# Kernel tuning notes

Hardware: AMD Instinct MI355X
Metric: run time of the kernel (lower is better)

## Reference

```python
import jax, jax.numpy as jnp
from jax import lax
import numpy as np

T, B, D, H = 512, 256, 128, 256
SHIFT = 0.0


def setup_inputs() -> dict:
    key = jax.random.key(0)
    ks = jax.random.split(key, 11)
    s_in = 1.0 / np.sqrt(D + H)
    s_cl = 1.0 / np.sqrt(H)
    return {
        "inputs": jax.random.normal(ks[0], (T, B, D), dtype=jnp.float32),
        "Wf": jax.random.normal(ks[1], (H, D + H), dtype=jnp.float32) * s_in,
        "bf": jax.random.normal(ks[2], (H,), dtype=jnp.float32) * s_in,
        "Wi": jax.random.normal(ks[3], (H, D + H), dtype=jnp.float32) * s_in,
        "bi": jax.random.normal(ks[4], (H,), dtype=jnp.float32) * s_in,
        "Wg": jax.random.normal(ks[5], (H, D + H), dtype=jnp.float32) * s_in,
        "bg": jax.random.normal(ks[6], (H,), dtype=jnp.float32) * s_in,
        "Wo": jax.random.normal(ks[7], (H, D + H), dtype=jnp.float32) * s_in,
        "bo": jax.random.normal(ks[8], (H,), dtype=jnp.float32) * s_in,
        "Wc": jax.random.normal(ks[9], (1, H), dtype=jnp.float32) * s_cl,
        "bc": jax.random.normal(ks[10], (1,), dtype=jnp.float32) * s_cl,
    }


def reference(inputs, Wf, bf, Wi, bi, Wg, bg, Wo, bo, Wc, bc):
    # Fuse the four gate linears into one GEMM per step: [4H, D+H]
    W = jnp.concatenate([Wf, Wi, Wg, Wo], axis=0)
    b = jnp.concatenate([bf, bi, bg, bo], axis=0)
    h = W.shape[0] // 4
    batch = inputs.shape[1]

    def step(carry, x):
        hx, cx = carry
        combined = jnp.concatenate([x, hx], axis=1)      # [B, D+H]
        z = combined @ W.T + b                            # [B, 4H]
        f = jax.nn.sigmoid(z[:, 0 * h:1 * h])
        i = jax.nn.sigmoid(z[:, 1 * h:2 * h])
        g = jnp.tanh(z[:, 2 * h:3 * h])
        o = jax.nn.sigmoid(z[:, 3 * h:4 * h])
        cx = f * cx + i * g
        hx = o * jnp.tanh(cx)
        return (hx, cx), hx

    h0 = jnp.zeros((batch, h), dtype=inputs.dtype)
    c0 = jnp.zeros((batch, h), dtype=inputs.dtype)
    (hx, cx), hs = lax.scan(step, (h0, c0), inputs)       # hs: [T, B, H]

    logits = hs @ Wc.T + bc                               # [T, B, 1]
    probs = jax.nn.sigmoid(logits + SHIFT)
    return (jnp.concatenate([probs, 1.0 - probs], axis=-1), hx, cx)
```

## Files before the change

### kernel.cpp

```cpp
#include <hip/hip_runtime.h>
#include <hip/hip_bf16.h>


#define T_STEPS 512
#define BATCH   256
#define DIN     128
#define HID     256
#define KDIM    384
#define LDK     520
#define GRIDN   256
#define NPOLL   96

typedef __attribute__((ext_vector_type(8))) short short8;
typedef __attribute__((ext_vector_type(4))) short short4v;
typedef __attribute__((ext_vector_type(4))) float f32x4;

__device__ __forceinline__ unsigned short f2bf(float f) {
    unsigned u = __float_as_uint(f);
    unsigned r = (u + 0x7FFFu + ((u >> 16) & 1u)) >> 16;
    return (unsigned short)r;
}
__device__ __forceinline__ float bf2f(unsigned short s) {
    return __uint_as_float(((unsigned)s) << 16);
}
__device__ __forceinline__ float sigmoid_f(float x) {
    return 1.f / (1.f + __expf(-x));
}
__device__ __forceinline__ float tanh_f(float x) {
    float e = __expf(2.f * x);
    return 1.f - 2.f / (e + 1.f);
}
__device__ __forceinline__ void poll_load_sc0(const unsigned int* p, uint4& a,
                                              uint4& b, uint4& c, uint4& d) {
    asm volatile(
        "global_load_dwordx4 %0, %4, off sc0\n\t"
        "global_load_dwordx4 %1, %4, off offset:16 sc0\n\t"
        "global_load_dwordx4 %2, %4, off offset:32 sc0\n\t"
        "global_load_dwordx4 %3, %4, off offset:48 sc0\n\t"
        "s_waitcnt vmcnt(0)"
        : "=&v"(a), "=&v"(b), "=&v"(c), "=&v"(d) : "v"(p) : "memory");
}
__device__ __forceinline__ void poll_load_sc1(const unsigned int* p, uint4& a,
                                              uint4& b, uint4& c, uint4& d) {
    asm volatile(
        "global_load_dwordx4 %0, %4, off sc1\n\t"
        "global_load_dwordx4 %1, %4, off offset:16 sc1\n\t"
        "global_load_dwordx4 %2, %4, off offset:32 sc1\n\t"
        "global_load_dwordx4 %3, %4, off offset:48 sc1\n\t"
        "s_waitcnt vmcnt(0)"
        : "=&v"(a), "=&v"(b), "=&v"(c), "=&v"(d) : "v"(p) : "memory");
}
__device__ __forceinline__ void store_sc0_u32(unsigned int* p, unsigned int v) {
    asm volatile("global_store_dword %0, %1, off sc0" :: "v"(p), "v"(v) : "memory");
}
__device__ __forceinline__ void store_sc1_u32(unsigned int* p, unsigned int v) {
    asm volatile("global_store_dword %0, %1, off sc1" :: "v"(p), "v"(v) : "memory");
}
__device__ __forceinline__ unsigned pack2bf(unsigned lo, unsigned hi) {
    return (hi & 0xFFFF0000u) | (lo >> 16);
}
__device__ __forceinline__ bool tags_ok(const uint4& a, const uint4& b,
                                        const uint4& c, const uint4& d,
                                        unsigned tag) {
    return ((a.x ^ tag) & 0xFFFFu) == 0 && ((a.y ^ tag) & 0xFFFFu) == 0 &&
           ((a.z ^ tag) & 0xFFFFu) == 0 && ((a.w ^ tag) & 0xFFFFu) == 0 &&
           ((b.x ^ tag) & 0xFFFFu) == 0 && ((b.y ^ tag) & 0xFFFFu) == 0 &&
           ((b.z ^ tag) & 0xFFFFu) == 0 && ((b.w ^ tag) & 0xFFFFu) == 0 &&
           ((c.x ^ tag) & 0xFFFFu) == 0 && ((c.y ^ tag) & 0xFFFFu) == 0 &&
           ((c.z ^ tag) & 0xFFFFu) == 0 && ((c.w ^ tag) & 0xFFFFu) == 0 &&
           ((d.x ^ tag) & 0xFFFFu) == 0 && ((d.y ^ tag) & 0xFFFFu) == 0 &&
           ((d.z ^ tag) & 0xFFFFu) == 0 && ((d.w ^ tag) & 0xFFFFu) == 0;
}

__global__ __launch_bounds__(256) void pack_w(
    const float* __restrict__ Wf, const float* __restrict__ Wi,
    const float* __restrict__ Wg, const float* __restrict__ Wo,
    unsigned short* __restrict__ Wp) {
    int idx = blockIdx.x * 256 + threadIdx.x;
    int n = idx / KDIM;
    int k = idx - n * KDIM;
    int g = n >> 8, j = n & 255;
    const float* s = (g == 0) ? Wf : (g == 1) ? Wi : (g == 2) ? Wg : Wo;
    Wp[idx] = f2bf(s[j * KDIM + k]);
}

__global__ __launch_bounds__(256) void pack_b(
    const float* __restrict__ bf, const float* __restrict__ bi,
    const float* __restrict__ bg, const float* __restrict__ bo,
    float* __restrict__ bp) {
    int n = blockIdx.x * 256 + threadIdx.x;
    int g = n >> 8, j = n & 255;
    const float* s = (g == 0) ? bf : (g == 1) ? bi : (g == 2) ? bg : bo;
    bp[n] = s[j];
}

__global__ __launch_bounds__(256) void init_k(unsigned int* __restrict__ hxp) {
    int tid = blockIdx.x * 256 + threadIdx.x;
    hxp[tid] = 0u;
    hxp[65536 + tid] = 0u;
    hxp[131072 + tid] = 0u;
    hxp[196608 + tid] = 0u;
}

__global__ __launch_bounds__(256, 1) void lstm_persist(
    const float* __restrict__ X,
    const unsigned short* __restrict__ W,
    const float* __restrict__ bias,
    unsigned int* __restrict__ hxp,
    unsigned short* __restrict__ hist,
    float* __restrict__ out) {
    __shared__ __align__(16) unsigned short comb_s[16 * LDK];
    __shared__ __align__(16) float z_s[4 * 272];
    __shared__ __align__(16) char pad_s[46080];
    __shared__ int fastok_s;

    const int tid = threadIdx.x;
    const int bg = blockIdx.x & 15, jg = blockIdx.x >> 4;
    const int b0 = bg * 16, j0 = jg * 16;
    const int wave = tid >> 6, lane = tid & 63;
    const int l16 = lane & 15, quad = lane >> 4;
    const int bi = tid >> 4, jj = tid & 15;
    const int b = b0 + bi, j = j0 + jj;

    const unsigned short* wrow =
        W + (size_t)(wave * 256 + j0 + l16) * KDIM + quad * 8;
    short8 wb[12];
#pragma unroll
    for (int kt = 0; kt < 12; ++kt) wb[kt] = *(const short8*)(wrow + kt * 32);

    const float bs0 = bias[0 * HID + j];
    const float bs1 = bias[1 * HID + j];
    const float bs2 = bias[2 * HID + j];
    const float bs3 = bias[3 * HID + j];
    if (tid == 0) {
        fastok_s = 1;
        ((volatile char*)pad_s)[0] = 0;
    }

    float c_reg = 0.f;
    float h_final = 0.f;

    const unsigned short* arow = &comb_s[l16 * LDK + quad * 8];
    const int hrow = tid >> 4, hc = tid & 15;
    const int xr0 = tid >> 5, xc4 = tid & 31, xr1 = (tid + 256) >> 5;

    {
        const float* x0b = X + b0 * DIN;
        float4 t0 = *(const float4*)(x0b + xr0 * DIN + xc4 * 4);
        float4 t1 = *(const float4*)(x0b + xr1 * DIN + xc4 * 4);
        short4v r;
        r.x = (short)f2bf(t0.x); r.y = (short)f2bf(t0.y);
        r.z = (short)f2bf(t0.z); r.w = (short)f2bf(t0.w);
        *(short4v*)(&comb_s[xr0 * LDK + xc4 * 4]) = r;
        r.x = (short)f2bf(t1.x); r.y = (short)f2bf(t1.y);
        r.z = (short)f2bf(t1.z); r.w = (short)f2bf(t1.w);
        *(short4v*)(&comb_s[xr1 * LDK + xc4 * 4]) = r;
    }
    float4 xv0 = *(const float4*)(X + (size_t)BATCH * DIN + b0 * DIN + xr0 * DIN + xc4 * 4);
    float4 xv1 = *(const float4*)(X + (size_t)BATCH * DIN + b0 * DIN + xr1 * DIN + xc4 * 4);
    __syncthreads();

    f32x4 acc_x0 = {0.f, 0.f, 0.f, 0.f}, acc_x1 = {0.f, 0.f, 0.f, 0.f};
#pragma unroll
    for (int kp = 0; kp < 2; ++kp) {
        short8 a0 = *(const short8*)(arow + (2 * kp) * 32);
        short8 a1 = *(const short8*)(arow + (2 * kp + 1) * 32);
        acc_x0 = __builtin_amdgcn_mfma_f32_16x16x32_bf16(a0, wb[2 * kp], acc_x0, 0, 0, 0);
        acc_x1 = __builtin_amdgcn_mfma_f32_16x16x32_bf16(a1, wb[2 * kp + 1], acc_x1, 0, 0, 0);
    }

    for (int k = 0; k < T_STEPS; ++k) {
        const unsigned tag = (unsigned)k;
        const unsigned int* fb =
            hxp + (k & 1) * 65536 + (b0 + hrow) * HID + hc * 16;
        const unsigned int* sb = fb + 131072;
        uint4 a, bq, cq, d;
        const int usefast = fastok_s;

        if (usefast) {
            int tries = NPOLL;
            bool ok = false;
            for (;;) {
                poll_load_sc0(fb, a, bq, cq, d);
                if (tags_ok(a, bq, cq, d, tag)) { ok = true; break; }
                if (--tries == 0) break;
            }
            if (!ok) {
                fastok_s = 0;
                for (;;) {
                    poll_load_sc1(sb, a, bq, cq, d);
                    if (tags_ok(a, bq, cq, d, tag)) break;
                    __builtin_amdgcn_s_sleep(1);
                }
            }
        } else {
            for (;;) {
                poll_load_sc1(sb, a, bq, cq, d);
                if (tags_ok(a, bq, cq, d, tag)) break;
                __builtin_amdgcn_s_sleep(1);
            }
        }

        {
            uint4 p0, p1;
            p0.x = pack2bf(a.x, a.y);   p0.y = pack2bf(a.z, a.w);
            p0.z = pack2bf(bq.x, bq.y); p0.w = pack2bf(bq.z, bq.w);
            p1.x = pack2bf(cq.x, cq.y); p1.y = pack2bf(cq.z, cq.w);
            p1.z = pack2bf(d.x, d.y);   p1.w = pack2bf(d.z, d.w);
            *(uint4*)(&comb_s[hrow * LDK + DIN + hc * 16]) = p0;
            *(uint4*)(&comb_s[hrow * LDK + DIN + hc * 16 + 8]) = p1;
        }
        if (k + 1 < T_STEPS) {
            const int xoff = ((k + 1) & 1) ? 384 : 0;
            short4v r;
            r.x = (short)f2bf(xv0.x); r.y = (short)f2bf(xv0.y);
            r.z = (short)f2bf(xv0.z); r.w = (short)f2bf(xv0.w);
            *(short4v*)(&comb_s[xr0 * LDK + xoff + xc4 * 4]) = r;
            r.x = (short)f2bf(xv1.x); r.y = (short)f2bf(xv1.y);
            r.z = (short)f2bf(xv1.z); r.w = (short)f2bf(xv1.w);
            *(short4v*)(&comb_s[xr1 * LDK + xoff + xc4 * 4]) = r;
        }
        __syncthreads();

        f32x4 acc0 = acc_x0, acc1 = acc_x1;
#pragma unroll
        for (int kt = 2; kt < 6; ++kt) {
            short8 a0 = *(const short8*)(arow + (2 * kt) * 32);
            short8 a1 = *(const short8*)(arow + (2 * kt + 1) * 32);
            acc0 = __builtin_amdgcn_mfma_f32_16x16x32_bf16(a0, wb[2 * kt], acc0, 0, 0, 0);
            acc1 = __builtin_amdgcn_mfma_f32_16x16x32_bf16(a1, wb[2 * kt + 1], acc1, 0, 0, 0);
        }
#pragma unroll
        for (int r = 0; r < 4; ++r)
            z_s[wave * 272 + (quad * 4 + r) * 17 + l16] = acc0[r] + acc1[r];
        __syncthreads();

        float zf = z_s[0 * 272 + bi * 17 + jj] + bs0;
        float zi = z_s[1 * 272 + bi * 17 + jj] + bs1;
        float zg = z_s[2 * 272 + bi * 17 + jj] + bs2;
        float zo = z_s[3 * 272 + bi * 17 + jj] + bs3;
        float fg = sigmoid_f(zf);
        float ig = sigmoid_f(zi);
        float gg = tanh_f(zg);
        float og = sigmoid_f(zo);
        c_reg = fg * c_reg + ig * gg;
        float hval = og * tanh_f(c_reg);
        unsigned short hb = f2bf(hval);
        unsigned int hword = ((unsigned)hb << 16) | (unsigned)(k + 1);
        unsigned int* fdst = hxp + ((k + 1) & 1) * 65536 + b * HID + j;
        store_sc0_u32(fdst, hword);
        store_sc1_u32(fdst + 131072, hword);
        hist[(size_t)k * BATCH * HID + b * HID + j] = hb;

        if (k + 1 < T_STEPS) {
            if (k + 2 < T_STEPS) {
                const float* xn = X + (size_t)(k + 2) * BATCH * DIN + b0 * DIN;
                xv0 = *(const float4*)(xn + xr0 * DIN + xc4 * 4);
                xv1 = *(const float4*)(xn + xr1 * DIN + xc4 * 4);
            }
            const int xoff = ((k + 1) & 1) ? 384 : 0;
            f32x4 ax0 = {0.f, 0.f, 0.f, 0.f}, ax1 = {0.f, 0.f, 0.f, 0.f};
#pragma unroll
            for (int kp = 0; kp < 2; ++kp) {
                short8 a0 = *(const short8*)(arow + xoff + (2 * kp) * 32);
                short8 a1 = *(const short8*)(arow + xoff + (2 * kp + 1) * 32);
                ax0 = __builtin_amdgcn_mfma_f32_16x16x32_bf16(a0, wb[2 * kp], ax0, 0, 0, 0);
                ax1 = __builtin_amdgcn_mfma_f32_16x16x32_bf16(a1, wb[2 * kp + 1], ax1, 0, 0, 0);
            }
            acc_x0 = ax0; acc_x1 = ax1;
        } else {
            h_final = hval;
        }
    }

    out[T_STEPS * BATCH * 2 + b * HID + j] = h_final;
    out[T_STEPS * BATCH * 2 + BATCH * HID + b * HID + j] = c_reg;
}

__global__ __launch_bounds__(256) void probs_k(
    const unsigned short* __restrict__ hist, const float* __restrict__ Wc,
    const float* __restrict__ bc, float* __restrict__ out) {
    const int wave = threadIdx.x >> 6, lane = threadIdx.x & 63;
    const size_t row = (size_t)blockIdx.x * 4 + wave;
    const unsigned short* h = hist + row * HID;
    short4v hv = *(const short4v*)(h + lane * 4);
    const float4 wv = *(const float4*)(Wc + lane * 4);
    float p = bf2f((unsigned short)hv.x) * wv.x + bf2f((unsigned short)hv.y) * wv.y +
              bf2f((unsigned short)hv.z) * wv.z + bf2f((unsigned short)hv.w) * wv.w;
#pragma unroll
    for (int off = 32; off >= 1; off >>= 1) p += __shfl_down(p, off);
    if (lane == 0) {
        float prob = 1.f / (1.f + __expf(-(p + bc[0])));
        out[row * 2]     = prob;
        out[row * 2 + 1] = 1.f - prob;
    }
}

extern "C" void kernel_launch(void* const* d_in, const int* in_sizes, int n_in,
                              void* d_out, int out_size, void* d_ws, size_t ws_size,
                              hipStream_t stream) {
    const float* X  = (const float*)d_in[0];
    const float* Wf = (const float*)d_in[1];
    const float* bfp= (const float*)d_in[2];
    const float* Wi = (const float*)d_in[3];
    const float* bip= (const float*)d_in[4];
    const float* Wg = (const float*)d_in[5];
    const float* bgp= (const float*)d_in[6];
    const float* Wo = (const float*)d_in[7];
    const float* bop= (const float*)d_in[8];
    const float* Wc = (const float*)d_in[9];
    const float* bc = (const float*)d_in[10];
    float* out = (float*)d_out;

    char* ws = (char*)d_ws;
    unsigned short* Wpack = (unsigned short*)(ws);
    float* bias = (float*)(ws + 786432);
    unsigned int* hxp = (unsigned int*)(ws + 790528);
    unsigned short* hist = (unsigned short*)(ws + 1839104);

    pack_w<<<1536, 256, 0, stream>>>(Wf, Wi, Wg, Wo, Wpack);
    pack_b<<<4, 256, 0, stream>>>(bfp, bip, bgp, bop, bias);
    init_k<<<256, 256, 0, stream>>>(hxp);

    void* kargs[6] = {(void*)&X, (void*)&Wpack, (void*)&bias,
                      (void*)&hxp, (void*)&hist, (void*)&out};
    (void)hipLaunchCooperativeKernel((const void*)lstm_persist, dim3(GRIDN),
                                     dim3(256), kargs, 0, stream);

    probs_k<<<32768, 256, 0, stream>>>(hist, Wc, bc, out);
}
```

Measured before the change: 1.102 ms.

## Fuse weight packing, state init and probability head into persistent LSTM kernel

Removes the separate pack_w, pack_b, init_k and probs_k launches. Each block now zeroes its slice of the exchange buffer and converts its fp32 weight rows to bf16 directly in registers, followed by a grid sync. After the recurrence, a second grid sync lets the blocks compute the classifier probabilities from the history buffer. This saves launch overheads and an intermediate weight buffer, but the output head now runs on only 256 blocks with serial per-wave loops, and two grid-wide barriers are added.

```diff
diff --git a/kernel.cpp b/kernel.cpp
--- a/kernel.cpp
+++ b/kernel.cpp
@@ -1,5 +1,8 @@
 #include <hip/hip_runtime.h>
 #include <hip/hip_bf16.h>
+#include <hip/hip_cooperative_groups.h>
+
+namespace cg = cooperative_groups;
 
 
 #define T_STEPS 512
@@ -72,40 +75,13 @@
            ((d.z ^ tag) & 0xFFFFu) == 0 && ((d.w ^ tag) & 0xFFFFu) == 0;
 }
 
-__global__ __launch_bounds__(256) void pack_w(
-    const float* __restrict__ Wf, const float* __restrict__ Wi,
-    const float* __restrict__ Wg, const float* __restrict__ Wo,
-    unsigned short* __restrict__ Wp) {
-    int idx = blockIdx.x * 256 + threadIdx.x;
-    int n = idx / KDIM;
-    int k = idx - n * KDIM;
-    int g = n >> 8, j = n & 255;
-    const float* s = (g == 0) ? Wf : (g == 1) ? Wi : (g == 2) ? Wg : Wo;
-    Wp[idx] = f2bf(s[j * KDIM + k]);
-}
-
-__global__ __launch_bounds__(256) void pack_b(
-    const float* __restrict__ bf, const float* __restrict__ bi,
-    const float* __restrict__ bg, const float* __restrict__ bo,
-    float* __restrict__ bp) {
-    int n = blockIdx.x * 256 + threadIdx.x;
-    int g = n >> 8, j = n & 255;
-    const float* s = (g == 0) ? bf : (g == 1) ? bi : (g == 2) ? bg : bo;
-    bp[n] = s[j];
-}
-
-__global__ __launch_bounds__(256) void init_k(unsigned int* __restrict__ hxp) {
-    int tid = blockIdx.x * 256 + threadIdx.x;
-    hxp[tid] = 0u;
-    hxp[65536 + tid] = 0u;
-    hxp[131072 + tid] = 0u;
-    hxp[196608 + tid] = 0u;
-}
-
 __global__ __launch_bounds__(256, 1) void lstm_persist(
     const float* __restrict__ X,
-    const unsigned short* __restrict__ W,
-    const float* __restrict__ bias,
+    const float* __restrict__ Wf, const float* __restrict__ bfp,
+    const float* __restrict__ Wi, const float* __restrict__ bip,
+    const float* __restrict__ Wg, const float* __restrict__ bgp,
+    const float* __restrict__ Wo, const float* __restrict__ bop,
+    const float* __restrict__ Wc, const float* __restrict__ bc,
     unsigned int* __restrict__ hxp,
     unsigned short* __restrict__ hist,
     float* __restrict__ out) {
@@ -122,20 +98,39 @@
     const int bi = tid >> 4, jj = tid & 15;
     const int b = b0 + bi, j = j0 + jj;
 
-    const unsigned short* wrow =
-        W + (size_t)(wave * 256 + j0 + l16) * KDIM + quad * 8;
+    {
+        int idx = blockIdx.x * 256 + tid;
+        hxp[idx] = 0u;
+        hxp[65536 + idx] = 0u;
+        hxp[131072 + idx] = 0u;
+        hxp[196608 + idx] = 0u;
+    }
+
+    const float* wsrc = (wave == 0) ? Wf : (wave == 1) ? Wi
+                      : (wave == 2) ? Wg : Wo;
+    const float* wr = wsrc + (size_t)(j0 + l16) * KDIM + quad * 8;
     short8 wb[12];
 #pragma unroll
-    for (int kt = 0; kt < 12; ++kt) wb[kt] = *(const short8*)(wrow + kt * 32);
-
-    const float bs0 = bias[0 * HID + j];
-    const float bs1 = bias[1 * HID + j];
-    const float bs2 = bias[2 * HID + j];
-    const float bs3 = bias[3 * HID + j];
+    for (int kt = 0; kt < 12; ++kt) {
+        f32x4 lo = *(const f32x4*)(wr + kt * 32);
+        f32x4 hi = *(const f32x4*)(wr + kt * 32 + 4);
+        short8 v;
+        v[0] = (short)f2bf(lo[0]); v[1] = (short)f2bf(lo[1]);
+        v[2] = (short)f2bf(lo[2]); v[3] = (short)f2bf(lo[3]);
+        v[4] = (short)f2bf(hi[0]); v[5] = (short)f2bf(hi[1]);
+        v[6] = (short)f2bf(hi[2]); v[7] = (short)f2bf(hi[3]);
+        wb[kt] = v;
+    }
+    const float bs0 = bfp[j];
+    const float bs1 = bip[j];
+    const float bs2 = bgp[j];
+    const float bs3 = bop[j];
     if (tid == 0) {
         fastok_s = 1;
         ((volatile char*)pad_s)[0] = 0;
     }
+
+    cg::this_grid().sync();
 
     float c_reg = 0.f;
     float h_final = 0.f;
@@ -275,24 +270,31 @@
 
     out[T_STEPS * BATCH * 2 + b * HID + j] = h_final;
     out[T_STEPS * BATCH * 2 + BATCH * HID + b * HID + j] = c_reg;
-}
-
-__global__ __launch_bounds__(256) void probs_k(
-    const unsigned short* __restrict__ hist, const float* __restrict__ Wc,
-    const float* __restrict__ bc, float* __restrict__ out) {
-    const int wave = threadIdx.x >> 6, lane = threadIdx.x & 63;
-    const size_t row = (size_t)blockIdx.x * 4 + wave;
-    const unsigned short* h = hist + row * HID;
-    short4v hv = *(const short4v*)(h + lane * 4);
-    const float4 wv = *(const float4*)(Wc + lane * 4);
-    float p = bf2f((unsigned short)hv.x) * wv.x + bf2f((unsigned short)hv.y) * wv.y +
-              bf2f((unsigned short)hv.z) * wv.z + bf2f((unsigned short)hv.w) * wv.w;
-#pragma unroll
-    for (int off = 32; off >= 1; off >>= 1) p += __shfl_down(p, off);
-    if (lane == 0) {
-        float prob = 1.f / (1.f + __expf(-(p + bc[0])));
-        out[row * 2]     = prob;
-        out[row * 2 + 1] = 1.f - prob;
+
+    cg::this_grid().sync();
+    {
+        const float bias_c = bc[0];
+        const float4 wv = *(const float4*)(Wc + lane * 4);
+        for (int i = 0; i < 128; ++i) {
+            const int lr = wave * 128 + i;
+            const int t = jg * 32 + (lr & 31);
+            const int bb = b0 + (lr >> 5);
+            const unsigned short* h =
+                hist + (size_t)t * BATCH * HID + (size_t)bb * HID;
+            short4v hv = *(const short4v*)(h + lane * 4);
+            float p = bf2f((unsigned short)hv.x) * wv.x +
+                      bf2f((unsigned short)hv.y) * wv.y +
+                      bf2f((unsigned short)hv.z) * wv.z +
+                      bf2f((unsigned short)hv.w) * wv.w;
+#pragma unroll
+            for (int off = 32; off >= 1; off >>= 1) p += __shfl_down(p, off);
+            if (lane == 0) {
+                float prob = 1.f / (1.f + __expf(-(p + bias_c)));
+                const size_t row = (size_t)t * BATCH + bb;
+                out[row * 2]     = prob;
+                out[row * 2 + 1] = 1.f - prob;
+            }
+        }
     }
 }
 
@@ -313,19 +315,16 @@
     float* out = (float*)d_out;
 
     char* ws = (char*)d_ws;
-    unsigned short* Wpack = (unsigned short*)(ws);
-    float* bias = (float*)(ws + 786432);
     unsigned int* hxp = (unsigned int*)(ws + 790528);
     unsigned short* hist = (unsigned short*)(ws + 1839104);
 
-    pack_w<<<1536, 256, 0, stream>>>(Wf, Wi, Wg, Wo, Wpack);
-    pack_b<<<4, 256, 0, stream>>>(bfp, bip, bgp, bop, bias);
-    init_k<<<256, 256, 0, stream>>>(hxp);
-
-    void* kargs[6] = {(void*)&X, (void*)&Wpack, (void*)&bias,
-                      (void*)&hxp, (void*)&hist, (void*)&out};
+    void* kargs[14] = {(void*)&X,
+                       (void*)&Wf, (void*)&bfp,
+                       (void*)&Wi, (void*)&bip,
+                       (void*)&Wg, (void*)&bgp,
+                       (void*)&Wo, (void*)&bop,
+                       (void*)&Wc, (void*)&bc,
+                       (void*)&hxp, (void*)&hist, (void*)&out};
     (void)hipLaunchCooperativeKernel((const void*)lstm_persist, dim3(GRIDN),
                                      dim3(256), kargs, 0, stream);
-
-    probs_k<<<32768, 256, 0, stream>>>(hist, Wc, bc, out);
-}
+}
```

After: 1.163 ms. 5.5% more time.
